# Optimization experiments

Hardware: AMD Instinct MI355X
Metric: run time of the kernel (lower is better)

The kernel has to match this reference:

```python
import jax, jax.numpy as jnp
import numpy as np

SUB_NO = 20
E_NO = 2000
I_NO = 500
T_NO = 200
M_NO = 8
B_NO = 12
T_DATA = 50000


def _binary_tree_cden(sub_no):
    C = np.zeros((sub_no, sub_no), np.float32)
    for p in range(sub_no):
        for c in (2 * p + 1, 2 * p + 2):
            if c < sub_no:
                C[p, c] = 1.0
    return jnp.asarray(C)


def _syn_assign(n_syn, sub_no):
    # one-hot synapse -> subunit assignment, [sub_no, n_syn]
    return jax.nn.one_hot(jnp.arange(n_syn) % sub_no, sub_no, dtype=jnp.float32).T


def setup_inputs() -> dict:
    key = jax.random.key(0)
    ks = jax.random.split(key, 12)
    S_e = jax.random.uniform(ks[0], (T_DATA, E_NO), jnp.float32)
    S_i = jax.random.uniform(ks[1], (T_DATA, I_NO), jnp.float32)
    # parameters (scaled randn so tanh/exp stay in a sane range)
    conv1_e_bases = jax.random.normal(ks[2], (B_NO, T_NO), jnp.float32)
    conv1_e_weights = 0.001 * jax.random.normal(ks[3], (M_NO * SUB_NO, B_NO), jnp.float32)
    conv1_i_bases = jax.random.normal(ks[4], (B_NO, T_NO), jnp.float32)
    conv1_i_weights = 0.001 * jax.random.normal(ks[5], (M_NO * SUB_NO, B_NO), jnp.float32)
    conv2_bases = jax.random.normal(ks[6], (B_NO, T_NO), jnp.float32)
    conv2_weights = 0.05 * jax.random.normal(ks[7], (M_NO * SUB_NO, B_NO), jnp.float32)
    leaf_linear = 0.3 * jax.random.normal(ks[8], (SUB_NO, M_NO), jnp.float32)
    multiplex_linear = 0.3 * jax.random.normal(ks[9], (SUB_NO, M_NO), jnp.float32)
    multiplex_bias = 0.3 * jax.random.normal(ks[10], (SUB_NO,), jnp.float32)
    return {
        "S_e": S_e, "S_i": S_i,
        "C_den": _binary_tree_cden(SUB_NO),
        "C_syn_e": _syn_assign(E_NO, SUB_NO),
        "C_syn_i": _syn_assign(I_NO, SUB_NO),
        "conv1_e_bases": conv1_e_bases, "conv1_e_weights": conv1_e_weights,
        "conv1_i_bases": conv1_i_bases, "conv1_i_weights": conv1_i_weights,
        "conv2_bases": conv2_bases, "conv2_weights": conv2_weights,
        "leaf_linear": leaf_linear, "multiplex_linear": multiplex_linear,
        "multiplex_bias": multiplex_bias,
    }


def _causal_conv1d(x, w, groups):
    # x: [1, C_in, T], w: [C_out, C_in/groups, K]; left-pad K-1 -> causal
    K = w.shape[-1]
    return jax.lax.conv_general_dilated(
        x, w, window_strides=(1,), padding=[(K - 1, 0)],
        feature_group_count=groups)


def reference(S_e, S_i, C_den, C_syn_e, C_syn_i,
              conv1_e_bases, conv1_e_weights, conv1_i_bases, conv1_i_weights,
              conv2_bases, conv2_weights, leaf_linear, multiplex_linear,
              multiplex_bias):
    T = S_e.shape[0]
    sub_no, M = multiplex_linear.shape
    # route synapses to subunits: [1, sub_no, T]
    Se = (S_e @ C_syn_e.T).T[None]
    Si = (S_i @ C_syn_i.T).T[None]
    # low-rank kernels: [M*sub_no, 1, T_no]
    k1e = (conv1_e_weights @ conv1_e_bases)[:, None, :]
    k1i = (conv1_i_weights @ conv1_i_bases)[:, None, :]
    k2 = (conv2_weights @ conv2_bases)[:, None, :]
    # grouped causal conv (groups = sub_no, M outputs per group)
    e1 = _causal_conv1d(Se, k1e, sub_no)[0].T.reshape(T, sub_no, M)
    i1 = _causal_conv1d(Si, k1i, sub_no)[0].T.reshape(T, sub_no, M)
    S_conv = e1 + i1  # [T, sub_no, M]
    expL = jnp.exp(leaf_linear)      # [sub_no, M]
    expM = jnp.exp(multiplex_linear)  # [sub_no, M]
    sub_out = jnp.zeros((T, sub_no), S_e.dtype)
    # reverse order: children (larger indices) computed before parents;
    # masked matmul == torch's gather of leaf children (zeros where C_den[p]==0)
    for p in range(sub_no - 1, -1, -1):
        leaf_in = (sub_out * C_den[p][None, :]) @ expL  # [T, M]
        h = jnp.tanh(S_conv[:, p, :] + leaf_in)         # [T, M]
        c2 = _causal_conv1d(h.T[None], k2[p * M:(p + 1) * M], M)[0].T  # depthwise
        g = jnp.tanh(c2)
        sub_out = sub_out.at[:, p].set(g @ expM[p] + multiplex_bias[p])
    return sub_out[:, 0]
```

## Files before the change

kernel.cpp:

```cpp
#include <hip/hip_runtime.h>
#include <math.h>

#define T_DATA 50000
#define E_NO   2000
#define I_NO   500
#define SUBN   20
#define MN     8
#define KLEN   200
#define TILE   512
#define HALO   199
#define TW     712

__device__ __forceinline__ float fast_tanh(float x) {
  float ax = fabsf(x);
  float e  = __expf(-2.f * ax);
  float r  = __builtin_amdgcn_rcpf(1.f + e);
  float t  = fmaf(-2.f * e, r, 1.f);
  return copysignf(t, x);
}

__device__ __forceinline__ void conv4(float acc[4], const float4 L,
                                      const float4 H, const float4 k4) {
  const float w0 = L.x, w1 = L.y, w2 = L.z, w3 = L.w;
  const float w4 = H.x, w5 = H.y, w6 = H.z;
  acc[0] += k4.x * w3; acc[1] += k4.x * w4; acc[2] += k4.x * w5; acc[3] += k4.x * w6;
  acc[0] += k4.y * w2; acc[1] += k4.y * w3; acc[2] += k4.y * w4; acc[3] += k4.y * w5;
  acc[0] += k4.z * w1; acc[1] += k4.z * w2; acc[2] += k4.z * w3; acc[3] += k4.z * w4;
  acc[0] += k4.w * w0; acc[1] += k4.w * w1; acc[2] += k4.w * w2; acc[3] += k4.w * w3;
}

__global__ __launch_bounds__(320) void route_kernel(
    const float* __restrict__ S_e, const float* __restrict__ S_i,
    float* __restrict__ Se, float* __restrict__ Si,
    const float* __restrict__ we, const float* __restrict__ be,
    const float* __restrict__ wi, const float* __restrict__ bi,
    const float* __restrict__ w2, const float* __restrict__ b2,
    float* __restrict__ k1e, float* __restrict__ k1i, float* __restrict__ k2) {
  __shared__ float lds_e[1280];
  __shared__ float lds_i[500];
  int tid = threadIdx.x;
  int bid = blockIdx.x;

  if (bid >= 12500) {
    int idx = (bid - 12500) * 320 + tid;
    if (idx < 160 * KLEN) {
      int row = idx / KLEN, d = idx % KLEN;
      int col = KLEN - 1 - d;
      float se = 0.f, si = 0.f, s2 = 0.f;
#pragma unroll
      for (int b = 0; b < 12; ++b) {
        se += we[row * 12 + b] * be[b * KLEN + col];
        si += wi[row * 12 + b] * bi[b * KLEN + col];
        s2 += w2[row * 12 + b] * b2[b * KLEN + col];
      }
      k1e[idx] = se; k1i[idx] = si; k2[idx] = s2;
    }
    return;
  }

  int t0 = bid * 4;
  for (int tt = 0; tt < 4; ++tt) {
    int t = t0 + tt;
    const float4* rowE = (const float4*)(S_e + (size_t)t * E_NO);
    float4 a = rowE[tid];
    if (tid < 180) {
      float4 b = rowE[tid + 320];
      a.x += b.x; a.y += b.y; a.z += b.z; a.w += b.w;
    }
    ((float4*)lds_e)[tid] = a;
    if (tid < 125) {
      const float4* rowI = (const float4*)(S_i + (size_t)t * I_NO);
      ((float4*)lds_i)[tid] = rowI[tid];
    }
    __syncthreads();
    if (tid < 20) {
      float s = 0.f;
#pragma unroll
      for (int k = 0; k < 64; ++k) s += lds_e[tid + 20 * k];
      Se[tid * T_DATA + t] = s;
    } else if (tid >= 64 && tid < 84) {
      int r = tid - 64;
      float s = 0.f;
#pragma unroll
      for (int k = 0; k < 25; ++k) s += lds_i[r + 20 * k];
      Si[r * T_DATA + t] = s;
    }
    __syncthreads();
  }
}

__global__ __launch_bounds__(256) void conv1_kernel(
    const float* __restrict__ Se, const float* __restrict__ Si,
    const float* __restrict__ k1e, const float* __restrict__ k1i,
    float* __restrict__ Sconv) {
  __shared__ float xe_raw[TW + 4], xi_raw[TW + 4];
  __shared__ float ke[MN * KLEN], ki[MN * KLEN];
  float* xe = xe_raw + 4;
  float* xi = xi_raw + 4;
  int s = blockIdx.y;
  int t0 = blockIdx.x * TILE;
  int tid = threadIdx.x;

  for (int idx = tid; idx < TW; idx += 256) {
    int t = t0 - HALO + idx;
    bool ok = (t >= 0) && (t < T_DATA) && (idx < 711);
    xe[idx] = ok ? Se[s * T_DATA + t] : 0.f;
    xi[idx] = ok ? Si[s * T_DATA + t] : 0.f;
  }
  for (int idx = tid; idx < MN * KLEN; idx += 256) {
    ke[idx] = k1e[s * MN * KLEN + idx];
    ki[idx] = k1i[s * MN * KLEN + idx];
  }
  __syncthreads();

  int m = tid >> 5, g = tid & 31;
  const float* kem = ke + m * KLEN;
  const float* kim = ki + m * KLEN;
  float* outp = Sconv + ((size_t)(s * MN + m)) * T_DATA + t0;

#pragma unroll 1
  for (int i = 0; i < 4; ++i) {
    const int U = 4 * g + 128 * i;
    const int S0 = U + 196;
    float4 Le = *(const float4*)(xe + S0);
    float4 He = *(const float4*)(xe + S0 + 4);
    float4 Lx = *(const float4*)(xi + S0);
    float4 Hx = *(const float4*)(xi + S0 + 4);
    float acc[4] = {0.f, 0.f, 0.f, 0.f};
    for (int d0 = 0; d0 < KLEN; d0 += 8) {
      float4 ka = *(const float4*)(kem + d0);
      float4 kb = *(const float4*)(kim + d0);
      conv4(acc, Le, He, ka);
      conv4(acc, Lx, Hx, kb);
      float4 Ne = *(const float4*)(xe + S0 - d0 - 4);
      float4 Nx = *(const float4*)(xi + S0 - d0 - 4);
      ka = *(const float4*)(kem + d0 + 4);
      kb = *(const float4*)(kim + d0 + 4);
      conv4(acc, Ne, Le, ka);
      conv4(acc, Nx, Lx, kb);
      He = Ne; Le = *(const float4*)(xe + S0 - d0 - 8);
      Hx = Nx; Lx = *(const float4*)(xi + S0 - d0 - 8);
    }
    if (t0 + U < T_DATA)
      *(float4*)(outp + U) = make_float4(acc[0], acc[1], acc[2], acc[3]);
  }
}

struct LevelArgs {
  int node[8];
  int c1[8];
  int c2[8];
};

template <int LT>
__global__ __launch_bounds__(256) void level_kernel(
    const float* __restrict__ Sconv, const float* __restrict__ k2r,
    const float* __restrict__ leaf_lin, const float* __restrict__ mult_lin,
    const float* __restrict__ mult_bias, float* __restrict__ sub_out,
    float* __restrict__ d_out, LevelArgs args) {
  const int TWL = LT + KLEN;
  __shared__ float hbuf_raw[4 + MN * (LT + KLEN)];
  __shared__ float k2l[MN * KLEN];
  __shared__ float red[MN * LT];
  float* hbuf = hbuf_raw + 4;
  int tid = threadIdx.x;
  int t0 = blockIdx.x * LT;
  int ni = blockIdx.y;
  int p = args.node[ni], c1 = args.c1[ni], c2 = args.c2[ni];

  for (int idx = tid; idx < MN * KLEN; idx += 256)
    k2l[idx] = k2r[p * MN * KLEN + idx];

  for (int m = 0; m < MN; ++m) {
    float eL1 = (c1 >= 0) ? __expf(leaf_lin[c1 * MN + m]) : 0.f;
    float eL2 = (c2 >= 0) ? __expf(leaf_lin[c2 * MN + m]) : 0.f;
    const float* scp = Sconv + ((size_t)(p * MN + m)) * T_DATA;
    const float* s1 = sub_out + (size_t)((c1 >= 0) ? c1 : 0) * T_DATA;
    const float* s2 = sub_out + (size_t)((c2 >= 0) ? c2 : 0) * T_DATA;
    for (int idx = tid; idx < TWL; idx += 256) {
      int t = t0 - HALO + idx;
      float v = 0.f;
      if (t >= 0 && t < T_DATA && idx < TWL - 1) {
        float x = scp[t];
        if (c1 >= 0) x += eL1 * s1[t];
        if (c2 >= 0) x += eL2 * s2[t];
        v = fast_tanh(x);
      }
      hbuf[m * TWL + idx] = v;
    }
  }
  __syncthreads();

  int m = tid >> 5, g = tid & 31;
  const float* km = k2l + m * KLEN;
  const float* hm = hbuf + m * TWL;
  float eM = __expf(mult_lin[p * MN + m]);

#pragma unroll 1
  for (int i = 0; i < LT / 128; ++i) {
    const int U = 4 * g + 128 * i;
    const int S0 = U + 196;
    float4 L = *(const float4*)(hm + S0);
    float4 H = *(const float4*)(hm + S0 + 4);
    float acc[4] = {0.f, 0.f, 0.f, 0.f};
    for (int d0 = 0; d0 < KLEN; d0 += 8) {
      float4 ka = *(const float4*)(km + d0);
      conv4(acc, L, H, ka);
      float4 N = *(const float4*)(hm + S0 - d0 - 4);
      ka = *(const float4*)(km + d0 + 4);
      conv4(acc, N, L, ka);
      H = N; L = *(const float4*)(hm + S0 - d0 - 8);
    }
    *(float4*)(red + m * LT + U) =
        make_float4(fast_tanh(acc[0]) * eM, fast_tanh(acc[1]) * eM,
                    fast_tanh(acc[2]) * eM, fast_tanh(acc[3]) * eM);
  }
  __syncthreads();

  float bias = mult_bias[p];
  float* outp = (p == 0) ? d_out : (sub_out + (size_t)p * T_DATA);
#pragma unroll
  for (int k = 0; k < (LT + 255) / 256; ++k) {
    int tl2 = tid + k * 256;
    if (tl2 < LT) {
      int t = t0 + tl2;
      if (t < T_DATA) {
        float ssum = bias;
#pragma unroll
        for (int mm = 0; mm < MN; ++mm) ssum += red[mm * LT + tl2];
        outp[t] = ssum;
      }
    }
  }
}

extern "C" void kernel_launch(void* const* d_in, const int* in_sizes, int n_in,
                              void* d_out, int out_size, void* d_ws, size_t ws_size,
                              hipStream_t stream) {
  const float* S_e  = (const float*)d_in[0];
  const float* S_i  = (const float*)d_in[1];
  const float* c1eb = (const float*)d_in[5];
  const float* c1ew = (const float*)d_in[6];
  const float* c1ib = (const float*)d_in[7];
  const float* c1iw = (const float*)d_in[8];
  const float* c2b  = (const float*)d_in[9];
  const float* c2w  = (const float*)d_in[10];
  const float* ll   = (const float*)d_in[11];
  const float* ml   = (const float*)d_in[12];
  const float* mb   = (const float*)d_in[13];

  float* ws    = (float*)d_ws;
  float* Se    = ws;
  float* Si    = ws + 1000000;
  float* Sconv = ws + 2000000;
  float* subo  = ws + 10000000;
  float* k1e   = ws + 11000000;
  float* k1i   = k1e + 32000;
  float* k2    = k1i + 32000;
  float* out   = (float*)d_out;

  route_kernel<<<dim3(12600), 320, 0, stream>>>(S_e, S_i, Se, Si,
                                                c1ew, c1eb, c1iw, c1ib, c2w, c2b,
                                                k1e, k1i, k2);

  conv1_kernel<<<dim3(98, SUBN), 256, 0, stream>>>(Se, Si, k1e, k1i, Sconv);

  LevelArgs L4 = {{15, 16, 17, 18, 19, 0, 0, 0},
                  {-1, -1, -1, -1, -1, 0, 0, 0},
                  {-1, -1, -1, -1, -1, 0, 0, 0}};
  LevelArgs L3 = {{7, 8, 9, 10, 11, 12, 13, 14},
                  {15, 17, 19, -1, -1, -1, -1, -1},
                  {16, 18, -1, -1, -1, -1, -1, -1}};
  LevelArgs L2 = {{3, 4, 5, 6, 0, 0, 0, 0},
                  {7, 9, 11, 13, 0, 0, 0, 0},
                  {8, 10, 12, 14, 0, 0, 0, 0}};
  LevelArgs L1 = {{1, 2, 0, 0, 0, 0, 0, 0},
                  {3, 5, 0, 0, 0, 0, 0, 0},
                  {4, 6, 0, 0, 0, 0, 0, 0}};
  LevelArgs L0 = {{0, 0, 0, 0, 0, 0, 0, 0},
                  {1, 0, 0, 0, 0, 0, 0, 0},
                  {2, 0, 0, 0, 0, 0, 0, 0}};

  level_kernel<256><<<dim3(196, 5), 256, 0, stream>>>(Sconv, k2, ll, ml, mb, subo, out, L4);
  level_kernel<256><<<dim3(196, 8), 256, 0, stream>>>(Sconv, k2, ll, ml, mb, subo, out, L3);
  level_kernel<128><<<dim3(391, 4), 256, 0, stream>>>(Sconv, k2, ll, ml, mb, subo, out, L2);
  level_kernel<128><<<dim3(391, 2), 256, 0, stream>>>(Sconv, k2, ll, ml, mb, subo, out, L1);
  level_kernel<128><<<dim3(391, 1), 256, 0, stream>>>(Sconv, k2, ll, ml, mb, subo, out, L0);
}
```

Baseline: 1.005 ms.

## Batch route reduction across timesteps, interleave conv tiles, rebalance tree levels

The route kernel now stages four timesteps into shared memory behind a single barrier. The per-subunit sums are spread over 320 threads with shuffle reductions, instead of 20-thread serial loops separated by two barriers per timestep. The conv1 and level kernels interleave their output tiles inside the tap loop, so kernel taps are loaded once per tap step and independent accumulators give more instruction-level parallelism, at the cost of more registers. The tree schedule moves leaf nodes 10-14 into the first level launch, leaving fewer nodes in the second launch.

```diff
diff --git a/kernel.cpp b/kernel.cpp
--- a/kernel.cpp
+++ b/kernel.cpp
@@ -36,8 +36,8 @@
     const float* __restrict__ wi, const float* __restrict__ bi,
     const float* __restrict__ w2, const float* __restrict__ b2,
     float* __restrict__ k1e, float* __restrict__ k1i, float* __restrict__ k2) {
-  __shared__ float lds_e[1280];
-  __shared__ float lds_i[500];
+  __shared__ float lds_e[4 * 1280];
+  __shared__ float lds_i[4 * 500];
   int tid = threadIdx.x;
   int bid = blockIdx.x;
 
@@ -59,6 +59,7 @@
   }
 
   int t0 = bid * 4;
+#pragma unroll
   for (int tt = 0; tt < 4; ++tt) {
     int t = t0 + tt;
     const float4* rowE = (const float4*)(S_e + (size_t)t * E_NO);
@@ -67,26 +68,31 @@
       float4 b = rowE[tid + 320];
       a.x += b.x; a.y += b.y; a.z += b.z; a.w += b.w;
     }
-    ((float4*)lds_e)[tid] = a;
+    ((float4*)(lds_e + tt * 1280))[tid] = a;
     if (tid < 125) {
       const float4* rowI = (const float4*)(S_i + (size_t)t * I_NO);
-      ((float4*)lds_i)[tid] = rowI[tid];
-    }
-    __syncthreads();
-    if (tid < 20) {
-      float s = 0.f;
-#pragma unroll
-      for (int k = 0; k < 64; ++k) s += lds_e[tid + 20 * k];
-      Se[tid * T_DATA + t] = s;
-    } else if (tid >= 64 && tid < 84) {
-      int r = tid - 64;
-      float s = 0.f;
-#pragma unroll
-      for (int k = 0; k < 25; ++k) s += lds_i[r + 20 * k];
-      Si[r * T_DATA + t] = s;
-    }
-    __syncthreads();
-  }
+      ((float4*)(lds_i + tt * 500))[tid] = rowI[tid];
+    }
+  }
+  __syncthreads();
+
+  int p = tid >> 2, j = tid & 3;
+  int tt = p / 20, s = p % 20;
+  const float* le = lds_e + tt * 1280 + s;
+  const float* li = lds_i + tt * 500 + s;
+  float se = 0.f;
+#pragma unroll
+  for (int i = 0; i < 16; ++i) se += le[20 * (4 * i + j)];
+  float sv = 0.f;
+#pragma unroll
+  for (int i = 0; i < 7; ++i) {
+    int k = 4 * i + j;
+    if (k < 25) sv += li[20 * k];
+  }
+  se += __shfl_xor(se, 1); se += __shfl_xor(se, 2);
+  sv += __shfl_xor(sv, 1); sv += __shfl_xor(sv, 2);
+  if (j == 0)      Se[s * T_DATA + t0 + tt] = se;
+  else if (j == 1) Si[s * T_DATA + t0 + tt] = sv;
 }
 
 __global__ __launch_bounds__(256) void conv1_kernel(
@@ -118,38 +124,49 @@
   const float* kim = ki + m * KLEN;
   float* outp = Sconv + ((size_t)(s * MN + m)) * T_DATA + t0;
 
-#pragma unroll 1
+  float4 Le[4], He[4], Lx[4], Hx[4];
+  float acc[4][4];
+#pragma unroll
+  for (int i = 0; i < 4; ++i) {
+    const int S0 = 4 * g + 128 * i + 196;
+    Le[i] = *(const float4*)(xe + S0);
+    He[i] = *(const float4*)(xe + S0 + 4);
+    Lx[i] = *(const float4*)(xi + S0);
+    Hx[i] = *(const float4*)(xi + S0 + 4);
+    acc[i][0] = acc[i][1] = acc[i][2] = acc[i][3] = 0.f;
+  }
+
+  for (int d0 = 0; d0 < KLEN; d0 += 8) {
+    float4 ka0 = *(const float4*)(kem + d0);
+    float4 kb0 = *(const float4*)(kim + d0);
+    float4 ka1 = *(const float4*)(kem + d0 + 4);
+    float4 kb1 = *(const float4*)(kim + d0 + 4);
+#pragma unroll
+    for (int i = 0; i < 4; ++i) {
+      const int S0 = 4 * g + 128 * i + 196;
+      conv4(acc[i], Le[i], He[i], ka0);
+      conv4(acc[i], Lx[i], Hx[i], kb0);
+      float4 Ne = *(const float4*)(xe + S0 - d0 - 4);
+      float4 Nx = *(const float4*)(xi + S0 - d0 - 4);
+      conv4(acc[i], Ne, Le[i], ka1);
+      conv4(acc[i], Nx, Lx[i], kb1);
+      He[i] = Ne; Le[i] = *(const float4*)(xe + S0 - d0 - 8);
+      Hx[i] = Nx; Lx[i] = *(const float4*)(xi + S0 - d0 - 8);
+    }
+  }
+
+#pragma unroll
   for (int i = 0; i < 4; ++i) {
     const int U = 4 * g + 128 * i;
-    const int S0 = U + 196;
-    float4 Le = *(const float4*)(xe + S0);
-    float4 He = *(const float4*)(xe + S0 + 4);
-    float4 Lx = *(const float4*)(xi + S0);
-    float4 Hx = *(const float4*)(xi + S0 + 4);
-    float acc[4] = {0.f, 0.f, 0.f, 0.f};
-    for (int d0 = 0; d0 < KLEN; d0 += 8) {
-      float4 ka = *(const float4*)(kem + d0);
-      float4 kb = *(const float4*)(kim + d0);
-      conv4(acc, Le, He, ka);
-      conv4(acc, Lx, Hx, kb);
-      float4 Ne = *(const float4*)(xe + S0 - d0 - 4);
-      float4 Nx = *(const float4*)(xi + S0 - d0 - 4);
-      ka = *(const float4*)(kem + d0 + 4);
-      kb = *(const float4*)(kim + d0 + 4);
-      conv4(acc, Ne, Le, ka);
-      conv4(acc, Nx, Lx, kb);
-      He = Ne; Le = *(const float4*)(xe + S0 - d0 - 8);
-      Hx = Nx; Lx = *(const float4*)(xi + S0 - d0 - 8);
-    }
     if (t0 + U < T_DATA)
-      *(float4*)(outp + U) = make_float4(acc[0], acc[1], acc[2], acc[3]);
+      *(float4*)(outp + U) = make_float4(acc[i][0], acc[i][1], acc[i][2], acc[i][3]);
   }
 }
 
 struct LevelArgs {
-  int node[8];
-  int c1[8];
-  int c2[8];
+  int node[10];
+  int c1[10];
+  int c2[10];
 };
 
 template <int LT>
@@ -159,6 +176,7 @@
     const float* __restrict__ mult_bias, float* __restrict__ sub_out,
     float* __restrict__ d_out, LevelArgs args) {
   const int TWL = LT + KLEN;
+  constexpr int NT = LT / 128;
   __shared__ float hbuf_raw[4 + MN * (LT + KLEN)];
   __shared__ float k2l[MN * KLEN];
   __shared__ float red[MN * LT];
@@ -196,24 +214,33 @@
   const float* hm = hbuf + m * TWL;
   float eM = __expf(mult_lin[p * MN + m]);
 
-#pragma unroll 1
-  for (int i = 0; i < LT / 128; ++i) {
+  float4 L[NT], H[NT];
+  float acc[NT][4];
+#pragma unroll
+  for (int i = 0; i < NT; ++i) {
+    const int S0 = 4 * g + 128 * i + 196;
+    L[i] = *(const float4*)(hm + S0);
+    H[i] = *(const float4*)(hm + S0 + 4);
+    acc[i][0] = acc[i][1] = acc[i][2] = acc[i][3] = 0.f;
+  }
+  for (int d0 = 0; d0 < KLEN; d0 += 8) {
+    float4 ka0 = *(const float4*)(km + d0);
+    float4 ka1 = *(const float4*)(km + d0 + 4);
+#pragma unroll
+    for (int i = 0; i < NT; ++i) {
+      const int S0 = 4 * g + 128 * i + 196;
+      conv4(acc[i], L[i], H[i], ka0);
+      float4 N = *(const float4*)(hm + S0 - d0 - 4);
+      conv4(acc[i], N, L[i], ka1);
+      H[i] = N; L[i] = *(const float4*)(hm + S0 - d0 - 8);
+    }
+  }
+#pragma unroll
+  for (int i = 0; i < NT; ++i) {
     const int U = 4 * g + 128 * i;
-    const int S0 = U + 196;
-    float4 L = *(const float4*)(hm + S0);
-    float4 H = *(const float4*)(hm + S0 + 4);
-    float acc[4] = {0.f, 0.f, 0.f, 0.f};
-    for (int d0 = 0; d0 < KLEN; d0 += 8) {
-      float4 ka = *(const float4*)(km + d0);
-      conv4(acc, L, H, ka);
-      float4 N = *(const float4*)(hm + S0 - d0 - 4);
-      ka = *(const float4*)(km + d0 + 4);
-      conv4(acc, N, L, ka);
-      H = N; L = *(const float4*)(hm + S0 - d0 - 8);
-    }
     *(float4*)(red + m * LT + U) =
-        make_float4(fast_tanh(acc[0]) * eM, fast_tanh(acc[1]) * eM,
-                    fast_tanh(acc[2]) * eM, fast_tanh(acc[3]) * eM);
+        make_float4(fast_tanh(acc[i][0]) * eM, fast_tanh(acc[i][1]) * eM,
+                    fast_tanh(acc[i][2]) * eM, fast_tanh(acc[i][3]) * eM);
   }
   __syncthreads();
 
@@ -265,25 +292,25 @@
 
   conv1_kernel<<<dim3(98, SUBN), 256, 0, stream>>>(Se, Si, k1e, k1i, Sconv);
 
-  LevelArgs L4 = {{15, 16, 17, 18, 19, 0, 0, 0},
-                  {-1, -1, -1, -1, -1, 0, 0, 0},
-                  {-1, -1, -1, -1, -1, 0, 0, 0}};
-  LevelArgs L3 = {{7, 8, 9, 10, 11, 12, 13, 14},
-                  {15, 17, 19, -1, -1, -1, -1, -1},
-                  {16, 18, -1, -1, -1, -1, -1, -1}};
-  LevelArgs L2 = {{3, 4, 5, 6, 0, 0, 0, 0},
-                  {7, 9, 11, 13, 0, 0, 0, 0},
-                  {8, 10, 12, 14, 0, 0, 0, 0}};
-  LevelArgs L1 = {{1, 2, 0, 0, 0, 0, 0, 0},
-                  {3, 5, 0, 0, 0, 0, 0, 0},
-                  {4, 6, 0, 0, 0, 0, 0, 0}};
-  LevelArgs L0 = {{0, 0, 0, 0, 0, 0, 0, 0},
-                  {1, 0, 0, 0, 0, 0, 0, 0},
-                  {2, 0, 0, 0, 0, 0, 0, 0}};
-
-  level_kernel<256><<<dim3(196, 5), 256, 0, stream>>>(Sconv, k2, ll, ml, mb, subo, out, L4);
-  level_kernel<256><<<dim3(196, 8), 256, 0, stream>>>(Sconv, k2, ll, ml, mb, subo, out, L3);
-  level_kernel<128><<<dim3(391, 4), 256, 0, stream>>>(Sconv, k2, ll, ml, mb, subo, out, L2);
-  level_kernel<128><<<dim3(391, 2), 256, 0, stream>>>(Sconv, k2, ll, ml, mb, subo, out, L1);
-  level_kernel<128><<<dim3(391, 1), 256, 0, stream>>>(Sconv, k2, ll, ml, mb, subo, out, L0);
-}
+  LevelArgs LA = {{10, 11, 12, 13, 14, 15, 16, 17, 18, 19},
+                  {-1, -1, -1, -1, -1, -1, -1, -1, -1, -1},
+                  {-1, -1, -1, -1, -1, -1, -1, -1, -1, -1}};
+  LevelArgs LB = {{7, 8, 9, 0, 0, 0, 0, 0, 0, 0},
+                  {15, 17, 19, 0, 0, 0, 0, 0, 0, 0},
+                  {16, 18, -1, 0, 0, 0, 0, 0, 0, 0}};
+  LevelArgs LC = {{3, 4, 5, 6, 0, 0, 0, 0, 0, 0},
+                  {7, 9, 11, 13, 0, 0, 0, 0, 0, 0},
+                  {8, 10, 12, 14, 0, 0, 0, 0, 0, 0}};
+  LevelArgs LD = {{1, 2, 0, 0, 0, 0, 0, 0, 0, 0},
+                  {3, 5, 0, 0, 0, 0, 0, 0, 0, 0},
+                  {4, 6, 0, 0, 0, 0, 0, 0, 0, 0}};
+  LevelArgs LE = {{0, 0, 0, 0, 0, 0, 0, 0, 0, 0},
+                  {1, 0, 0, 0, 0, 0, 0, 0, 0, 0},
+                  {2, 0, 0, 0, 0, 0, 0, 0, 0, 0}};
+
+  level_kernel<256><<<dim3(196, 10), 256, 0, stream>>>(Sconv, k2, ll, ml, mb, subo, out, LA);
+  level_kernel<256><<<dim3(196, 3),  256, 0, stream>>>(Sconv, k2, ll, ml, mb, subo, out, LB);
+  level_kernel<128><<<dim3(391, 4),  256, 0, stream>>>(Sconv, k2, ll, ml, mb, subo, out, LC);
+  level_kernel<128><<<dim3(391, 2),  256, 0, stream>>>(Sconv, k2, ll, ml, mb, subo, out, LD);
+  level_kernel<128><<<dim3(391, 1),  256, 0, stream>>>(Sconv, k2, ll, ml, mb, subo, out, LE);
+}
```

Measured after the change: 0.9996 ms. About the same (-0.6%).
